# Kernel tuning notes

Hardware: AMD Instinct MI355X
Metric: run time of the kernel (lower is better)

## Reference

```python
import jax, jax.numpy as jnp
import numpy as np


def setup_inputs() -> dict:
    key = jax.random.key(0)
    ks = jax.random.split(key, 10)
    B, T = 64, 2048
    inp_p, inp_q, out = 512, 512, 512
    def xavier(k, shape):
        fan_in, fan_out = shape[1], shape[0]
        limit = np.sqrt(6.0 / (fan_in + fan_out))
        return jax.random.uniform(k, shape, jnp.float32, -limit, limit)
    return {
        "input_p": jax.random.normal(ks[0], (B, inp_p), jnp.float32),
        "input_q": jax.random.normal(ks[1], (B, T, inp_q), jnp.float32),
        "h_tm1": jax.random.normal(ks[2], (B, out), jnp.float32),
        "Wp": xavier(ks[3], (out, inp_p)),
        "bp": jnp.zeros((out,), jnp.float32),
        "Wq": xavier(ks[4], (out, inp_q)),
        "bq": jnp.zeros((out,), jnp.float32),
        "Wr": xavier(ks[5], (out, out)),
        "br": jnp.zeros((out,), jnp.float32),
        "w": 0.05 * jax.random.normal(ks[6], (out,), jnp.float32),
        "match_b": jnp.ones((1,), jnp.float32),
        "depth": 0,
    }


def reference(input_p, input_q, h_tm1, Wp, bp, Wq, bq, Wr, br, w, match_b, depth):
    # depth selects the layer; single layer (depth=0) parameters provided.
    G_p = (input_p @ Wp.T + bp)[:, None, :]          # [B, 1, out]
    G_q = jnp.einsum("btq,oq->bto", input_q, Wq) + bq  # [B, T, out]
    G_r = (h_tm1 @ Wr.T + br)[:, None, :]            # [B, 1, out]
    G = jnp.tanh(G_p + G_q + G_r)                    # [B, T, out]
    alpha = jnp.einsum("bto,o->bt", G, w) + match_b[0]  # [B, T]
    alpha = jax.nn.softmax(alpha, axis=-1)
    z = jnp.einsum("bt,btq->bq", alpha, input_q)     # [B, inp_q]
    return jnp.concatenate([input_p, z], axis=1)     # [B, inp_p+inp_q]
```

## Files before the change

### kernel.cpp

```cpp
#include <hip/hip_runtime.h>
#include <hip/hip_bf16.h>
#include <stdint.h>
#include <stddef.h>


typedef __attribute__((ext_vector_type(8))) short short8;
typedef __attribute__((ext_vector_type(8))) unsigned short ushort8v;
typedef __attribute__((ext_vector_type(4))) float f32x4;

__device__ __forceinline__ unsigned short f2bf(float f) {
    unsigned int u = __builtin_bit_cast(unsigned int, f);
    return (unsigned short)((u + 0x7FFFu + ((u >> 16) & 1u)) >> 16);
}

__device__ __forceinline__ void gload_lds16(const void* g, void* l) {
    __builtin_amdgcn_global_load_lds(
        (const __attribute__((address_space(1))) unsigned int*)g,
        (__attribute__((address_space(3))) unsigned int*)l, 16, 0, 0);
}

__device__ __forceinline__ short8 cvt8(float4 a, float4 b) {
    union { __hip_bfloat162 h[4]; short8 s; } u;
    u.h[0] = __float22bfloat162_rn(make_float2(a.x, a.y));
    u.h[1] = __float22bfloat162_rn(make_float2(a.z, a.w));
    u.h[2] = __float22bfloat162_rn(make_float2(b.x, b.y));
    u.h[3] = __float22bfloat162_rn(make_float2(b.z, b.w));
    return u.s;
}

__global__ __launch_bounds__(256) void k_zero(float* __restrict__ p) {
    int i = (blockIdx.x * 256 + threadIdx.x) * 4;
    *(float4*)(p + i) = make_float4(0.f, 0.f, 0.f, 0.f);
}

__global__ __launch_bounds__(256) void k_convert(const float* __restrict__ Wq,
                                                 unsigned short* __restrict__ Wq_bf) {
    int i = (blockIdx.x * 256 + threadIdx.x) * 8;
    float4 a = *(const float4*)(Wq + i);
    float4 b = *(const float4*)(Wq + i + 4);
    ushort8v o;
    o[0] = f2bf(a.x); o[1] = f2bf(a.y); o[2] = f2bf(a.z); o[3] = f2bf(a.w);
    o[4] = f2bf(b.x); o[5] = f2bf(b.y); o[6] = f2bf(b.z); o[7] = f2bf(b.w);
    *(ushort8v*)(Wq_bf + i) = o;
}

__global__ __launch_bounds__(256) void k_prq(
        const float* __restrict__ ip, const float* __restrict__ h,
        const float* __restrict__ Wp, const float* __restrict__ Wr,
        const float* __restrict__ bp, const float* __restrict__ bq,
        const float* __restrict__ br, float* __restrict__ prq) {
    __shared__ float ip_lds[64][68];
    __shared__ float h_lds[64][68];
    __shared__ float wp_lds[8][68];
    __shared__ float wr_lds[8][68];
    const int tid = threadIdx.x;
    const int o0 = blockIdx.x * 8;
    const int bb = tid >> 3;
    const int oo = tid & 7;
    float acc0 = 0.f, acc1 = 0.f;
    const int lrow = tid >> 2;
    const int lcol = (tid & 3) * 16;
    for (int kc = 0; kc < 512; kc += 64) {
        #pragma unroll
        for (int j = 0; j < 16; j += 4) {
            float4 v = *(const float4*)(ip + lrow * 512 + kc + lcol + j);
            ip_lds[lrow][lcol + j] = v.x; ip_lds[lrow][lcol + j + 1] = v.y;
            ip_lds[lrow][lcol + j + 2] = v.z; ip_lds[lrow][lcol + j + 3] = v.w;
            float4 u = *(const float4*)(h + lrow * 512 + kc + lcol + j);
            h_lds[lrow][lcol + j] = u.x; h_lds[lrow][lcol + j + 1] = u.y;
            h_lds[lrow][lcol + j + 2] = u.z; h_lds[lrow][lcol + j + 3] = u.w;
        }
        if (tid < 128) {
            int r = tid >> 4, c = (tid & 15) * 4;
            float4 v = *(const float4*)(Wp + (size_t)(o0 + r) * 512 + kc + c);
            wp_lds[r][c] = v.x; wp_lds[r][c + 1] = v.y; wp_lds[r][c + 2] = v.z; wp_lds[r][c + 3] = v.w;
        } else {
            int t2 = tid - 128;
            int r = t2 >> 4, c = (t2 & 15) * 4;
            float4 v = *(const float4*)(Wr + (size_t)(o0 + r) * 512 + kc + c);
            wr_lds[r][c] = v.x; wr_lds[r][c + 1] = v.y; wr_lds[r][c + 2] = v.z; wr_lds[r][c + 3] = v.w;
        }
        __syncthreads();
        #pragma unroll 4
        for (int k = 0; k < 64; ++k) {
            float wpv = wp_lds[oo][k], wrv = wr_lds[oo][k];
            acc0 += ip_lds[bb][k] * wpv + h_lds[bb][k] * wrv;
            acc1 += ip_lds[bb + 32][k] * wpv + h_lds[bb + 32][k] * wrv;
        }
        __syncthreads();
    }
    const int o = o0 + oo;
    float base = bp[o] + bq[o] + br[o];
    prq[bb * 512 + o] = acc0 + base;
    prq[(bb + 32) * 512 + o] = acc1 + base;
}

__global__ __launch_bounds__(256, 3) void k_gq(
        const float* __restrict__ iq, const unsigned short* __restrict__ Wq_bf,
        const float* __restrict__ prq, const float* __restrict__ wv,
        float* __restrict__ logits) {
    __shared__ unsigned short A2[2][4096];
    __shared__ unsigned short B2[2][4096];
    __shared__ float w_lds[128];
    __shared__ float prq_lds[128];
    __shared__ float red[2][128];

    const int tid = threadIdx.x;
    const int bid = blockIdx.x;
    const int orig = (bid & 7) * 512 + (bid >> 3);
    const int m0 = (orig >> 2) * 128;
    const int n0 = (orig & 3) * 128;
    const int b = m0 >> 11;

    if (tid < 128) {
        w_lds[tid] = wv[n0 + tid];
        prq_lds[tid] = prq[b * 512 + n0 + tid];
    }

    const int lane = tid & 63;
    const int wave = tid >> 6;
    const int wm = wave >> 1;
    const int wn = wave & 1;
    const int r16 = lane & 15;
    const int cc = lane >> 4;
    const int swz = ((cc ^ ((r16 >> 1) & 3)) << 3);

    const int ar0 = tid >> 2, ac0 = tid & 3;
    const int ar1 = 64 + (tid >> 2), ac1 = tid & 3;
    const float* asrc0 = iq + (size_t)(m0 + ar0) * 512 + ac0 * 8;
    const float* asrc1 = iq + (size_t)(m0 + ar1) * 512 + ac1 * 8;
    const int aoff0 = ar0 * 32 + ((ac0 ^ ((ar0 >> 1) & 3)) << 3);
    const int aoff1 = ar1 * 32 + ((ac1 ^ ((ar1 >> 1) & 3)) << 3);

    const int brw0 = tid >> 2, bs0 = (tid & 3) ^ ((brw0 >> 1) & 3);
    const int brw1 = 64 + (tid >> 2);
    const int bs1 = (tid & 3) ^ ((brw1 >> 1) & 3);
    const unsigned short* bsrc0 = Wq_bf + (size_t)(n0 + brw0) * 512 + (bs0 << 3);
    const unsigned short* bsrc1 = Wq_bf + (size_t)(n0 + brw1) * 512 + (bs1 << 3);

    f32x4 acc[4][4];
    #pragma unroll
    for (int i = 0; i < 4; ++i)
        #pragma unroll
        for (int j = 0; j < 4; ++j) acc[i][j] = (f32x4){0.f, 0.f, 0.f, 0.f};

    float4 ra0, ra1, ra2, ra3;

    gload_lds16(bsrc0, (char*)&B2[0][0] + wave * 1024);
    gload_lds16(bsrc1, (char*)&B2[0][0] + 4096 + wave * 1024);
    ra0 = *(const float4*)(asrc0);
    ra1 = *(const float4*)(asrc0 + 4);
    ra2 = *(const float4*)(asrc1);
    ra3 = *(const float4*)(asrc1 + 4);
    *(short8*)&A2[0][aoff0] = cvt8(ra0, ra1);
    *(short8*)&A2[0][aoff1] = cvt8(ra2, ra3);
    asm volatile("s_waitcnt vmcnt(0) lgkmcnt(0)" ::: "memory");
    __builtin_amdgcn_sched_barrier(0);
    __builtin_amdgcn_s_barrier();

#define PHASE(K, C, PF)                                                          \
    {                                                                            \
        if (PF) {                                                                \
            gload_lds16(bsrc0 + (K) + 32, (char*)&B2[(C) ^ 1][0] + wave * 1024); \
            gload_lds16(bsrc1 + (K) + 32, (char*)&B2[(C) ^ 1][0] + 4096 + wave * 1024); \
            ra0 = *(const float4*)(asrc0 + (K) + 32);                            \
            ra1 = *(const float4*)(asrc0 + (K) + 36);                            \
            ra2 = *(const float4*)(asrc1 + (K) + 32);                            \
            ra3 = *(const float4*)(asrc1 + (K) + 36);                            \
        }                                                                        \
        short8 af0 = *(const short8*)&A2[C][(wm * 64 +  0 + r16) * 32 + swz];    \
        short8 af1 = *(const short8*)&A2[C][(wm * 64 + 16 + r16) * 32 + swz];    \
        short8 af2 = *(const short8*)&A2[C][(wm * 64 + 32 + r16) * 32 + swz];    \
        short8 af3 = *(const short8*)&A2[C][(wm * 64 + 48 + r16) * 32 + swz];    \
        _Pragma("unroll")                                                        \
        for (int nf = 0; nf < 4; ++nf) {                                         \
            short8 bfr = *(const short8*)&B2[C][(wn * 64 + nf * 16 + r16) * 32 + swz]; \
            acc[0][nf] = __builtin_amdgcn_mfma_f32_16x16x32_bf16(af0, bfr, acc[0][nf], 0, 0, 0); \
            acc[1][nf] = __builtin_amdgcn_mfma_f32_16x16x32_bf16(af1, bfr, acc[1][nf], 0, 0, 0); \
            acc[2][nf] = __builtin_amdgcn_mfma_f32_16x16x32_bf16(af2, bfr, acc[2][nf], 0, 0, 0); \
            acc[3][nf] = __builtin_amdgcn_mfma_f32_16x16x32_bf16(af3, bfr, acc[3][nf], 0, 0, 0); \
        }                                                                        \
        if (PF) {                                                                \
            *(short8*)&A2[(C) ^ 1][aoff0] = cvt8(ra0, ra1);                      \
            *(short8*)&A2[(C) ^ 1][aoff1] = cvt8(ra2, ra3);                      \
        }                                                                        \
        asm volatile("s_waitcnt vmcnt(0) lgkmcnt(0)" ::: "memory");              \
        __builtin_amdgcn_sched_barrier(0);                                       \
        __builtin_amdgcn_s_barrier();                                            \
    }

    for (int kk = 0; kk < 512; kk += 64) {
        PHASE(kk, 0, 1);
        PHASE(kk + 32, 1, (kk + 64) < 512);
    }
#undef PHASE

    float part[4][4];
    #pragma unroll
    for (int mf = 0; mf < 4; ++mf)
        #pragma unroll
        for (int j = 0; j < 4; ++j) part[mf][j] = 0.f;

    #pragma unroll
    for (int nf = 0; nf < 4; ++nf) {
        int c = wn * 64 + nf * 16 + r16;
        float wc = w_lds[c];
        float pc = prq_lds[c];
        #pragma unroll
        for (int mf = 0; mf < 4; ++mf) {
            #pragma unroll
            for (int j = 0; j < 4; ++j) {
                float x = acc[mf][nf][j] + pc;
                float e = __expf(2.f * x);
                part[mf][j] += wc * (1.f - 2.f / (e + 1.f));
            }
        }
    }
    #pragma unroll
    for (int mf = 0; mf < 4; ++mf)
        #pragma unroll
        for (int j = 0; j < 4; ++j) {
            float v = part[mf][j];
            v += __shfl_xor(v, 1);
            v += __shfl_xor(v, 2);
            v += __shfl_xor(v, 4);
            v += __shfl_xor(v, 8);
            part[mf][j] = v;
        }
    if (r16 == 0) {
        #pragma unroll
        for (int mf = 0; mf < 4; ++mf)
            #pragma unroll
            for (int j = 0; j < 4; ++j)
                red[wn][wm * 64 + mf * 16 + cc * 4 + j] = part[mf][j];
    }
    __syncthreads();
    if (tid < 128)
        atomicAdd(&logits[m0 + tid], red[0][tid] + red[1][tid]);
}

__global__ __launch_bounds__(256) void k_stats(const float* __restrict__ logits,
                                               const float* __restrict__ ip,
                                               float* __restrict__ out,
                                               float* __restrict__ stats) {
    const int b = blockIdx.x, tid = threadIdx.x;
    __shared__ float sm[256];
    float m = -1e30f;
    for (int i = tid; i < 2048; i += 256) m = fmaxf(m, logits[b * 2048 + i]);
    sm[tid] = m;
    __syncthreads();
    for (int s = 128; s > 0; s >>= 1) {
        if (tid < s) sm[tid] = fmaxf(sm[tid], sm[tid + s]);
        __syncthreads();
    }
    float bmax = sm[0];
    __syncthreads();
    float ssum = 0.f;
    for (int i = tid; i < 2048; i += 256) ssum += __expf(logits[b * 2048 + i] - bmax);
    sm[tid] = ssum;
    __syncthreads();
    for (int s = 128; s > 0; s >>= 1) {
        if (tid < s) sm[tid] += sm[tid + s];
        __syncthreads();
    }
    if (tid == 0) { stats[b * 2] = bmax; stats[b * 2 + 1] = sm[0]; }
    out[b * 1024 + tid] = ip[b * 512 + tid];
    out[b * 1024 + 256 + tid] = ip[b * 512 + 256 + tid];
    out[b * 1024 + 512 + tid] = 0.f;
    out[b * 1024 + 768 + tid] = 0.f;
}

#define TC 128
__global__ __launch_bounds__(256) void k_z(const float* __restrict__ logits,
                                           const float* __restrict__ stats,
                                           const float* __restrict__ iq,
                                           float* __restrict__ out) {
    const int blk = blockIdx.x;
    const int b = blk >> 4;
    const int c = blk & 15;
    const int tid = threadIdx.x;
    __shared__ float al[TC];
    const float bmax = stats[b * 2];
    const float inv = 1.f / stats[b * 2 + 1];
    if (tid < TC) al[tid] = __expf(logits[b * 2048 + c * TC + tid] - bmax) * inv;
    __syncthreads();
    const int q = tid * 2;
    float ax = 0.f, ay = 0.f;
    const float* base = iq + ((size_t)b * 2048 + (size_t)c * TC) * 512 + q;
    #pragma unroll 4
    for (int t = 0; t < TC; ++t) {
        float2 v = *(const float2*)(base + (size_t)t * 512);
        float a = al[t];
        ax += a * v.x;
        ay += a * v.y;
    }
    atomicAdd(&out[b * 1024 + 512 + q], ax);
    atomicAdd(&out[b * 1024 + 512 + q + 1], ay);
}

extern "C" void kernel_launch(void* const* d_in, const int* in_sizes, int n_in,
                              void* d_out, int out_size, void* d_ws, size_t ws_size,
                              hipStream_t stream) {
    const float* input_p = (const float*)d_in[0];
    const float* input_q = (const float*)d_in[1];
    const float* h_tm1   = (const float*)d_in[2];
    const float* Wp      = (const float*)d_in[3];
    const float* bp      = (const float*)d_in[4];
    const float* Wq      = (const float*)d_in[5];
    const float* bq      = (const float*)d_in[6];
    const float* Wr      = (const float*)d_in[7];
    const float* br      = (const float*)d_in[8];
    const float* wv      = (const float*)d_in[9];
    float* out = (float*)d_out;

    char* ws = (char*)d_ws;
    unsigned short* Wq_bf = (unsigned short*)ws;
    float* prq    = (float*)(ws + 512 * 1024);
    float* logits = (float*)(ws + 640 * 1024);
    float* stats  = (float*)(ws + 1152 * 1024);

    k_zero<<<dim3(128), dim3(256), 0, stream>>>(logits);
    k_convert<<<dim3(128), dim3(256), 0, stream>>>(Wq, Wq_bf);
    k_prq<<<dim3(64), dim3(256), 0, stream>>>(input_p, h_tm1, Wp, Wr, bp, bq, br, prq);
    k_gq<<<dim3(4096), dim3(256), 0, stream>>>(input_q, Wq_bf, prq, wv, logits);
    k_stats<<<dim3(64), dim3(256), 0, stream>>>(logits, input_p, out, stats);
    k_z<<<dim3(64 * 16), dim3(256), 0, stream>>>(logits, stats, input_q, out);
}
```

Measured before the change: 205.8 us.

## Pre-convert input_q to bf16 and run the GEMM and z-reduction on it

Adds a pass that converts the whole input_q tensor to bf16 in workspace. The logit GEMM then loads both operands directly into LDS with global_load_lds and a double-buffered pipeline, instead of converting fp32 in registers. The z weighted-sum kernel also reads the bf16 copy. The aim is to shrink per-kernel reads and drop in-loop conversion. The cost is an extra full read of fp32 input_q plus a write of the bf16 copy, and lower precision in the z output.

```diff
diff --git a/kernel.cpp b/kernel.cpp
--- a/kernel.cpp
+++ b/kernel.cpp
@@ -7,17 +7,6 @@
 typedef __attribute__((ext_vector_type(8))) short short8;
 typedef __attribute__((ext_vector_type(8))) unsigned short ushort8v;
 typedef __attribute__((ext_vector_type(4))) float f32x4;
-
-__device__ __forceinline__ unsigned short f2bf(float f) {
-    unsigned int u = __builtin_bit_cast(unsigned int, f);
-    return (unsigned short)((u + 0x7FFFu + ((u >> 16) & 1u)) >> 16);
-}
-
-__device__ __forceinline__ void gload_lds16(const void* g, void* l) {
-    __builtin_amdgcn_global_load_lds(
-        (const __attribute__((address_space(1))) unsigned int*)g,
-        (__attribute__((address_space(3))) unsigned int*)l, 16, 0, 0);
-}
 
 __device__ __forceinline__ short8 cvt8(float4 a, float4 b) {
     union { __hip_bfloat162 h[4]; short8 s; } u;
@@ -28,20 +17,28 @@
     return u.s;
 }
 
+__device__ __forceinline__ float bf2f(unsigned short u) {
+    unsigned v = (unsigned)u << 16;
+    return __builtin_bit_cast(float, v);
+}
+
+__device__ __forceinline__ void gload_lds16(const void* g, void* l) {
+    __builtin_amdgcn_global_load_lds(
+        (const __attribute__((address_space(1))) unsigned int*)g,
+        (__attribute__((address_space(3))) unsigned int*)l, 16, 0, 0);
+}
+
 __global__ __launch_bounds__(256) void k_zero(float* __restrict__ p) {
     int i = (blockIdx.x * 256 + threadIdx.x) * 4;
     *(float4*)(p + i) = make_float4(0.f, 0.f, 0.f, 0.f);
 }
 
-__global__ __launch_bounds__(256) void k_convert(const float* __restrict__ Wq,
-                                                 unsigned short* __restrict__ Wq_bf) {
-    int i = (blockIdx.x * 256 + threadIdx.x) * 8;
-    float4 a = *(const float4*)(Wq + i);
-    float4 b = *(const float4*)(Wq + i + 4);
-    ushort8v o;
-    o[0] = f2bf(a.x); o[1] = f2bf(a.y); o[2] = f2bf(a.z); o[3] = f2bf(a.w);
-    o[4] = f2bf(b.x); o[5] = f2bf(b.y); o[6] = f2bf(b.z); o[7] = f2bf(b.w);
-    *(ushort8v*)(Wq_bf + i) = o;
+__global__ __launch_bounds__(256) void k_convert8(const float* __restrict__ src,
+                                                  unsigned short* __restrict__ dst) {
+    size_t i = ((size_t)blockIdx.x * 256 + threadIdx.x) * 8;
+    float4 a = *(const float4*)(src + i);
+    float4 b = *(const float4*)(src + i + 4);
+    *(short8*)(dst + i) = cvt8(a, b);
 }
 
 __global__ __launch_bounds__(256) void k_prq(
@@ -95,7 +92,136 @@
     prq[(bb + 32) * 512 + o] = acc1 + base;
 }
 
-__global__ __launch_bounds__(256, 3) void k_gq(
+__global__ __launch_bounds__(256, 2) void k_gq16(
+        const unsigned short* __restrict__ iqb, const unsigned short* __restrict__ Wq_bf,
+        const float* __restrict__ prq, const float* __restrict__ wv,
+        float* __restrict__ logits) {
+    __shared__ unsigned short A2[2][4096];
+    __shared__ unsigned short B2[2][4096];
+    __shared__ float w_lds[128];
+    __shared__ float prq_lds[128];
+    __shared__ float red[2][128];
+
+    const int tid = threadIdx.x;
+    const int bid = blockIdx.x;
+    const int orig = (bid & 7) * 512 + (bid >> 3);
+    const int m0 = (orig >> 2) * 128;
+    const int n0 = (orig & 3) * 128;
+    const int b = m0 >> 11;
+
+    if (tid < 128) {
+        w_lds[tid] = wv[n0 + tid];
+        prq_lds[tid] = prq[b * 512 + n0 + tid];
+    }
+
+    const int lane = tid & 63;
+    const int wave = tid >> 6;
+    const int wm = wave >> 1;
+    const int wn = wave & 1;
+    const int r16 = lane & 15;
+    const int cc = lane >> 4;
+    const int swz = ((cc ^ ((r16 >> 1) & 3)) << 3);
+
+    const unsigned short *as0, *as1, *bs0, *bs1;
+    {
+        int t0 = tid, row0 = t0 >> 2, g0 = (t0 & 3) ^ ((row0 >> 1) & 3);
+        as0 = iqb + (size_t)(m0 + row0) * 512 + (g0 << 3);
+        bs0 = Wq_bf + (size_t)(n0 + row0) * 512 + (g0 << 3);
+        int t1 = 256 + tid, row1 = t1 >> 2, g1 = (t1 & 3) ^ ((row1 >> 1) & 3);
+        as1 = iqb + (size_t)(m0 + row1) * 512 + (g1 << 3);
+        bs1 = Wq_bf + (size_t)(n0 + row1) * 512 + (g1 << 3);
+    }
+    char* abase = (char*)A2;
+    char* bbase = (char*)B2;
+
+#define STAGE(K, BUF)                                                      \
+    {                                                                      \
+        gload_lds16(as0 + (K), abase + (BUF) * 8192 + wave * 1024);        \
+        gload_lds16(as1 + (K), abase + (BUF) * 8192 + 4096 + wave * 1024); \
+        gload_lds16(bs0 + (K), bbase + (BUF) * 8192 + wave * 1024);        \
+        gload_lds16(bs1 + (K), bbase + (BUF) * 8192 + 4096 + wave * 1024); \
+    }
+
+    f32x4 acc[4][4];
+    #pragma unroll
+    for (int i = 0; i < 4; ++i)
+        #pragma unroll
+        for (int j = 0; j < 4; ++j) acc[i][j] = (f32x4){0.f, 0.f, 0.f, 0.f};
+
+    STAGE(0, 0);
+    #pragma unroll 2
+    for (int s = 0; s < 16; ++s) {
+        if (s < 15) {
+            STAGE((s + 1) * 32, (s + 1) & 1);
+            asm volatile("s_waitcnt vmcnt(4)" ::: "memory");
+        } else {
+            asm volatile("s_waitcnt vmcnt(0)" ::: "memory");
+        }
+        __builtin_amdgcn_s_barrier();
+        const unsigned short* Ab = &A2[s & 1][0];
+        const unsigned short* Bb = &B2[s & 1][0];
+        short8 af0 = *(const short8*)&Ab[(wm * 64 +  0 + r16) * 32 + swz];
+        short8 af1 = *(const short8*)&Ab[(wm * 64 + 16 + r16) * 32 + swz];
+        short8 af2 = *(const short8*)&Ab[(wm * 64 + 32 + r16) * 32 + swz];
+        short8 af3 = *(const short8*)&Ab[(wm * 64 + 48 + r16) * 32 + swz];
+        #pragma unroll
+        for (int nf = 0; nf < 4; ++nf) {
+            short8 bfr = *(const short8*)&Bb[(wn * 64 + nf * 16 + r16) * 32 + swz];
+            acc[0][nf] = __builtin_amdgcn_mfma_f32_16x16x32_bf16(af0, bfr, acc[0][nf], 0, 0, 0);
+            acc[1][nf] = __builtin_amdgcn_mfma_f32_16x16x32_bf16(af1, bfr, acc[1][nf], 0, 0, 0);
+            acc[2][nf] = __builtin_amdgcn_mfma_f32_16x16x32_bf16(af2, bfr, acc[2][nf], 0, 0, 0);
+            acc[3][nf] = __builtin_amdgcn_mfma_f32_16x16x32_bf16(af3, bfr, acc[3][nf], 0, 0, 0);
+        }
+        asm volatile("s_waitcnt lgkmcnt(0)" ::: "memory");
+        __builtin_amdgcn_s_barrier();
+    }
+#undef STAGE
+
+    float part[4][4];
+    #pragma unroll
+    for (int mf = 0; mf < 4; ++mf)
+        #pragma unroll
+        for (int j = 0; j < 4; ++j) part[mf][j] = 0.f;
+
+    #pragma unroll
+    for (int nf = 0; nf < 4; ++nf) {
+        int c = wn * 64 + nf * 16 + r16;
+        float wc = w_lds[c];
+        float pc = prq_lds[c];
+        #pragma unroll
+        for (int mf = 0; mf < 4; ++mf) {
+            #pragma unroll
+            for (int j = 0; j < 4; ++j) {
+                float x = acc[mf][nf][j] + pc;
+                float e = __expf(2.f * x);
+                part[mf][j] += wc * (1.f - 2.f / (e + 1.f));
+            }
+        }
+    }
+    #pragma unroll
+    for (int mf = 0; mf < 4; ++mf)
+        #pragma unroll
+        for (int j = 0; j < 4; ++j) {
+            float v = part[mf][j];
+            v += __shfl_xor(v, 1);
+            v += __shfl_xor(v, 2);
+            v += __shfl_xor(v, 4);
+            v += __shfl_xor(v, 8);
+            part[mf][j] = v;
+        }
+    if (r16 == 0) {
+        #pragma unroll
+        for (int mf = 0; mf < 4; ++mf)
+            #pragma unroll
+            for (int j = 0; j < 4; ++j)
+                red[wn][wm * 64 + mf * 16 + cc * 4 + j] = part[mf][j];
+    }
+    __syncthreads();
+    if (tid < 128)
+        atomicAdd(&logits[m0 + tid], red[0][tid] + red[1][tid]);
+}
+
+__global__ __launch_bounds__(256, 3) void k_gq32(
         const float* __restrict__ iq, const unsigned short* __restrict__ Wq_bf,
         const float* __restrict__ prq, const float* __restrict__ wv,
         float* __restrict__ logits) {
@@ -132,11 +258,11 @@
     const int aoff0 = ar0 * 32 + ((ac0 ^ ((ar0 >> 1) & 3)) << 3);
     const int aoff1 = ar1 * 32 + ((ac1 ^ ((ar1 >> 1) & 3)) << 3);
 
-    const int brw0 = tid >> 2, bs0 = (tid & 3) ^ ((brw0 >> 1) & 3);
+    const int brw0 = tid >> 2, bsw0 = (tid & 3) ^ ((brw0 >> 1) & 3);
     const int brw1 = 64 + (tid >> 2);
-    const int bs1 = (tid & 3) ^ ((brw1 >> 1) & 3);
-    const unsigned short* bsrc0 = Wq_bf + (size_t)(n0 + brw0) * 512 + (bs0 << 3);
-    const unsigned short* bsrc1 = Wq_bf + (size_t)(n0 + brw1) * 512 + (bs1 << 3);
+    const int bsw1 = (tid & 3) ^ ((brw1 >> 1) & 3);
+    const unsigned short* bsrc0 = Wq_bf + (size_t)(n0 + brw0) * 512 + (bsw0 << 3);
+    const unsigned short* bsrc1 = Wq_bf + (size_t)(n0 + brw1) * 512 + (bsw1 << 3);
 
     f32x4 acc[4][4];
     #pragma unroll
@@ -271,10 +397,37 @@
 }
 
 #define TC 128
-__global__ __launch_bounds__(256) void k_z(const float* __restrict__ logits,
-                                           const float* __restrict__ stats,
-                                           const float* __restrict__ iq,
-                                           float* __restrict__ out) {
+__global__ __launch_bounds__(256) void k_z16(const float* __restrict__ logits,
+                                             const float* __restrict__ stats,
+                                             const unsigned short* __restrict__ iqb,
+                                             float* __restrict__ out) {
+    const int blk = blockIdx.x;
+    const int b = blk >> 4;
+    const int c = blk & 15;
+    const int tid = threadIdx.x;
+    __shared__ float al[TC];
+    const float bmax = stats[b * 2];
+    const float inv = 1.f / stats[b * 2 + 1];
+    if (tid < TC) al[tid] = __expf(logits[b * 2048 + c * TC + tid] - bmax) * inv;
+    __syncthreads();
+    const int q = tid * 2;
+    float ax = 0.f, ay = 0.f;
+    const unsigned short* base = iqb + ((size_t)b * 2048 + (size_t)c * TC) * 512 + q;
+    #pragma unroll 4
+    for (int t = 0; t < TC; ++t) {
+        ushort2 v = *(const ushort2*)(base + (size_t)t * 512);
+        float a = al[t];
+        ax += a * bf2f(v.x);
+        ay += a * bf2f(v.y);
+    }
+    atomicAdd(&out[b * 1024 + 512 + q], ax);
+    atomicAdd(&out[b * 1024 + 512 + q + 1], ay);
+}
+
+__global__ __launch_bounds__(256) void k_z32(const float* __restrict__ logits,
+                                             const float* __restrict__ stats,
+                                             const float* __restrict__ iq,
+                                             float* __restrict__ out) {
     const int blk = blockIdx.x;
     const int b = blk >> 4;
     const int c = blk & 15;
@@ -318,11 +471,22 @@
     float* prq    = (float*)(ws + 512 * 1024);
     float* logits = (float*)(ws + 640 * 1024);
     float* stats  = (float*)(ws + 1152 * 1024);
+    unsigned short* iq_bf = (unsigned short*)(ws + 2 * 1024 * 1024);
+
+    const size_t need = 2ull * 1024 * 1024 + 134217728ull;
 
     k_zero<<<dim3(128), dim3(256), 0, stream>>>(logits);
-    k_convert<<<dim3(128), dim3(256), 0, stream>>>(Wq, Wq_bf);
+    k_convert8<<<dim3(128), dim3(256), 0, stream>>>(Wq, Wq_bf);
     k_prq<<<dim3(64), dim3(256), 0, stream>>>(input_p, h_tm1, Wp, Wr, bp, bq, br, prq);
-    k_gq<<<dim3(4096), dim3(256), 0, stream>>>(input_q, Wq_bf, prq, wv, logits);
-    k_stats<<<dim3(64), dim3(256), 0, stream>>>(logits, input_p, out, stats);
-    k_z<<<dim3(64 * 16), dim3(256), 0, stream>>>(logits, stats, input_q, out);
-}
+
+    if (ws_size >= need) {
+        k_convert8<<<dim3(32768), dim3(256), 0, stream>>>(input_q, iq_bf);
+        k_gq16<<<dim3(4096), dim3(256), 0, stream>>>(iq_bf, Wq_bf, prq, wv, logits);
+        k_stats<<<dim3(64), dim3(256), 0, stream>>>(logits, input_p, out, stats);
+        k_z16<<<dim3(64 * 16), dim3(256), 0, stream>>>(logits, stats, iq_bf, out);
+    } else {
+        k_gq32<<<dim3(4096), dim3(256), 0, stream>>>(input_q, Wq_bf, prq, wv, logits);
+        k_stats<<<dim3(64), dim3(256), 0, stream>>>(logits, input_p, out, stats);
+        k_z32<<<dim3(64 * 16), dim3(256), 0, stream>>>(logits, stats, input_q, out);
+    }
+}
```

Result: slower. 231.2 us (+12.3%).
